# Performance work log

Measured on AMD Instinct MI355X. Metric: run time of the kernel, lower is better.

## Reference

```python
import jax, jax.numpy as jnp
import numpy as np
from jax import lax

# dims
B, CH, CC, DG, H, W = 2, 256, 256, 8, 64, 64
KK = 3  # dcn kernel size
K = KK * KK
GN_GROUPS = 32
EPS = 1e-6


def conv2d(x, w, b, pad=0, groups=1):
    out = lax.conv_general_dilated(x, w, (1, 1), [(pad, pad), (pad, pad)],
                                   feature_group_count=groups)
    return out + b[None, :, None, None]


def group_norm(x, gamma, beta):
    b, c, h, w = x.shape
    xg = x.reshape(b, GN_GROUPS, c // GN_GROUPS, h, w)
    mu = xg.mean(axis=(2, 3, 4), keepdims=True)
    var = xg.var(axis=(2, 3, 4), keepdims=True)
    xn = ((xg - mu) * lax.rsqrt(var + EPS)).reshape(b, c, h, w)
    return xn * gamma[None, :, None, None] + beta[None, :, None, None]


def deform_conv2d(x, off_y, off_x, mask, weight, bias):
    # x: [B,C,H,W]; off_y/off_x/mask: [B,DG,K,H,W]; weight: [Cout,C,3,3]
    b, c, h, w = x.shape
    cg = c // DG
    offs = jnp.arange(KK, dtype=x.dtype) - (KK // 2)  # pad = 1, dilation = 1
    ky = jnp.repeat(offs, KK)  # [K]
    kx = jnp.tile(offs, KK)    # [K]
    base_y = ky[:, None, None] + jnp.arange(h, dtype=x.dtype)[None, :, None]  # [K,H,1]
    base_x = kx[:, None, None] + jnp.arange(w, dtype=x.dtype)[None, None, :]  # [K,1,W]
    py = base_y[None, None] + off_y  # [B,DG,K,H,W]
    px = base_x[None, None] + off_x
    y0f = jnp.floor(py)
    x0f = jnp.floor(px)
    wy1 = py - y0f
    wx1 = px - x0f
    y0 = y0f.astype(jnp.int32)
    x0 = x0f.astype(jnp.int32)
    xg = x.reshape(b, DG, cg, h * w)

    def gather(yi, xi, wt):
        valid = (yi >= 0) & (yi < h) & (xi >= 0) & (xi < w)  # zero padding outside
        idx = (jnp.clip(yi, 0, h - 1) * w + jnp.clip(xi, 0, w - 1)).reshape(b, DG, 1, K * h * w)
        g = jnp.take_along_axis(xg, idx, axis=3).reshape(b, DG, cg, K, h, w)
        return g * (wt * valid)[:, :, None]

    val = (gather(y0, x0, (1 - wy1) * (1 - wx1))
           + gather(y0, x0 + 1, (1 - wy1) * wx1)
           + gather(y0 + 1, x0, wy1 * (1 - wx1))
           + gather(y0 + 1, x0 + 1, wy1 * wx1))
    val = val * mask[:, :, None]  # modulated (DCNv2)
    w_r = weight.reshape(weight.shape[0], DG, cg, K)
    out = jnp.einsum('bgckhw,ogck->bohw', val, w_r)
    return out + bias[None, :, None, None]


def setup_inputs():
    key = jax.random.key(0)
    ks = jax.random.split(key, 32)
    s = 0.02
    inp = {
        'x_main': jax.random.normal(ks[0], (B, CH, H, W), jnp.float32),
        'prior': jax.random.normal(ks[1], (B, CC, 2 * H, 2 * W), jnp.float32),
        # downsample (bilinear resize + 3x3 conv)
        'w_ds': s * jax.random.normal(ks[2], (CC, CC, 3, 3), jnp.float32),
        'b_ds': jnp.zeros((CC,), jnp.float32),
        # offset_conv1: 1x1 -> GN -> SiLU -> depthwise 7x7 -> GN -> SiLU -> 1x1
        'w1': s * jax.random.normal(ks[3], (CH, CH + CC, 1, 1), jnp.float32),
        'b1': jnp.zeros((CH,), jnp.float32),
        'g1': jnp.ones((CH,), jnp.float32),
        'bt1': jnp.zeros((CH,), jnp.float32),
        'w_dw': s * jax.random.normal(ks[4], (CH, 1, 7, 7), jnp.float32),
        'b_dw': jnp.zeros((CH,), jnp.float32),
        'g2': jnp.ones((CH,), jnp.float32),
        'bt2': jnp.zeros((CH,), jnp.float32),
        'w2': s * jax.random.normal(ks[5], (CH, CH, 1, 1), jnp.float32),
        'b2': jnp.zeros((CH,), jnp.float32),
        # offset_conv2: 3x3 -> GN -> SiLU
        'w3': s * jax.random.normal(ks[6], (CH, CH, 3, 3), jnp.float32),
        'b3': jnp.zeros((CH,), jnp.float32),
        'g3': jnp.ones((CH,), jnp.float32),
        'bt3': jnp.zeros((CH,), jnp.float32),
        # dcn.conv_offset: 3x3 -> 3*DG*K channels (small init -> small offsets)
        'w_off': 0.01 * jax.random.normal(ks[7], (3 * DG * K, CH, 3, 3), jnp.float32),
        'b_off': jnp.zeros((3 * DG * K,), jnp.float32),
        # dcn main weight
        'w_dcn': s * jax.random.normal(ks[8], (CH, CH, 3, 3), jnp.float32),
        'b_dcn': jnp.zeros((CH,), jnp.float32),
    }
    return inp


def reference(x_main, prior, w_ds, b_ds, w1, b1, g1, bt1, w_dw, b_dw, g2, bt2,
              w2, b2, w3, b3, g3, bt3, w_off, b_off, w_dcn, b_dcn):
    b, c, h, w = x_main.shape
    # downsample prior to x_main resolution (bilinear, align_corners=False) + 3x3 conv
    pr = jax.image.resize(prior, (b, prior.shape[1], h, w), method='bilinear')
    pr = conv2d(pr, w_ds, b_ds, pad=1)
    # offset_conv1
    t = conv2d(jnp.concatenate([pr, x_main], axis=1), w1, b1, pad=0)
    t = jax.nn.silu(group_norm(t, g1, bt1))
    t = conv2d(t, w_dw, b_dw, pad=3, groups=c)  # depthwise 7x7
    t = jax.nn.silu(group_norm(t, g2, bt2))
    t = conv2d(t, w2, b2, pad=0)
    # offset_conv2 (previous_offset is None)
    offset_feat = jax.nn.silu(group_norm(conv2d(t, w3, b3, pad=1), g3, bt3))
    # DCNv2Pack: offsets/mask from offset_feat, sample x_main
    o = conv2d(offset_feat, w_off, b_off, pad=1)  # [B, 3*DG*K, H, W]
    o1, o2, m = jnp.split(o, 3, axis=1)
    off = jnp.concatenate([o1, o2], axis=1).reshape(b, DG, K, 2, h, w)
    off_y = off[:, :, :, 0]
    off_x = off[:, :, :, 1]
    mask = jax.nn.sigmoid(m).reshape(b, DG, K, h, w)
    warp_feat = deform_conv2d(x_main, off_y, off_x, mask, w_dcn, b_dcn)
    return warp_feat, offset_feat
```

## Files before the change

### kernel.cpp

```cpp
#include <hip/hip_runtime.h>
#include <math.h>


typedef __attribute__((ext_vector_type(8))) short short8;
typedef __attribute__((ext_vector_type(4))) float f32x4;
typedef unsigned short ushort_t;
typedef unsigned int uint_t;

__device__ __forceinline__ ushort_t f2bf(float f) {
  uint_t u = __float_as_uint(f);
  return (ushort_t)((u + 0x7fffu + ((u >> 16) & 1u)) >> 16);
}
__device__ __forceinline__ float bf2f(ushort_t h) {
  return __uint_as_float(((uint_t)h) << 16);
}
__device__ __forceinline__ uint_t pk2(float a, float b) {
  return (uint_t)f2bf(a) | ((uint_t)f2bf(b) << 16);
}

#define GLL(g, l) \
  __builtin_amdgcn_global_load_lds((const __attribute__((address_space(1))) void*)(const void*)(g), \
                                   (__attribute__((address_space(3))) void*)(void*)(l), 16, 0, 0)
#define WAITVM(n) __builtin_amdgcn_s_waitcnt(0x0F70 | (n))
#define CFENCE() asm volatile("" ::: "memory")

#define OFF_P1   0u
#define OFF_Y1   4460544u
#define OFF_Y2   8654848u
#define OFF_O    12849152u
#define OFF_WDS  16388096u
#define OFF_W1   17567744u
#define OFF_W2   17829888u
#define OFF_W3   17960960u
#define OFF_X    19140608u
#define OFF_WDW  23334912u

__global__ __launch_bounds__(256) void k_down(const float* __restrict__ pr,
                                              ushort_t* __restrict__ out) {
  int idx = blockIdx.x * 256 + threadIdx.x;
  int x = idx & 63, y = (idx >> 6) & 63, bc = idx >> 12;
  const float* p = pr + (size_t)bc * 16384;
  const float w4[4] = {0.125f, 0.375f, 0.375f, 0.125f};
  float wy[4], wx[4];
  int ry[4], rx[4];
  float sy = 0.f, sx = 0.f;
#pragma unroll
  for (int t = 0; t < 4; ++t) {
    int yy = 2 * y - 1 + t;
    bool vy = (yy >= 0) && (yy < 128);
    wy[t] = vy ? w4[t] : 0.f; ry[t] = vy ? yy : 0; sy += wy[t];
    int xx = 2 * x - 1 + t;
    bool vx = (xx >= 0) && (xx < 128);
    wx[t] = vx ? w4[t] : 0.f; rx[t] = vx ? xx : 0; sx += wx[t];
  }
  float acc = 0.f;
#pragma unroll
  for (int t = 0; t < 4; ++t) {
    const float* rowp = p + ry[t] * 128;
    acc += wy[t] * (wx[0] * rowp[rx[0]] + wx[1] * rowp[rx[1]] +
                    wx[2] * rowp[rx[2]] + wx[3] * rowp[rx[3]]);
  }
  out[idx] = f2bf(acc / (sy * sx));
}

template <typename SrcT>
__global__ __launch_bounds__(256) void k_tr(const SrcT* __restrict__ src,
                                            ushort_t* __restrict__ dst,
                                            int pad) {
  __shared__ SrcT tile[64][65];
  int bx = blockIdx.x;
  int c4 = bx & 3, y = (bx >> 2) & 63, b = bx >> 8;
  int tid = threadIdx.x;
  int x = tid & 63, cl = tid >> 6;
#pragma unroll
  for (int i = 0; i < 16; ++i) {
    int c = (c4 << 6) + cl + (i << 2);
    tile[cl + (i << 2)][x] = src[(((size_t)(b * 256 + c)) << 12) + (y << 6) + x];
  }
  __syncthreads();
  int W = 64 + 2 * pad;
  int c2 = tid & 63, xq = tid >> 6;
#pragma unroll
  for (int i = 0; i < 16; ++i) {
    int x2 = xq + (i << 2);
    SrcT v = tile[c2][x2];
    ushort_t o;
    if constexpr (sizeof(SrcT) == 4) o = f2bf((float)v); else o = (ushort_t)v;
    dst[((size_t)((b * W + y + pad) * W + x2 + pad)) * 256 + (c4 << 6) + c2] = o;
  }
}

__global__ __launch_bounds__(256) void k_wprep_all(
    const float* __restrict__ w_ds, const float* __restrict__ w1,
    const float* __restrict__ w2, const float* __restrict__ w3,
    const float* __restrict__ w_dw,
    ushort_t* __restrict__ Wds, ushort_t* __restrict__ W1,
    ushort_t* __restrict__ W2, ushort_t* __restrict__ W3,
    float* __restrict__ Wdw) {
  int i = blockIdx.x * 256 + threadIdx.x;
  if (i < 589824) {
    int tap = i >> 16, r = i & 65535, co = r >> 8, ci = r & 255;
    Wds[i] = f2bf(w_ds[((co << 8) + ci) * 9 + tap]);
  } else if (i < 720896) {
    int l = i - 589824;
    W1[l] = f2bf(w1[l]);
  } else if (i < 786432) {
    int l = i - 720896;
    W2[l] = f2bf(w2[l]);
  } else if (i < 1376256) {
    int l = i - 786432;
    int tap = l >> 16, r = l & 65535, co = r >> 8, ci = r & 255;
    W3[l] = f2bf(w3[((co << 8) + ci) * 9 + tap]);
  } else if (i < 1388800) {
    int l = i - 1376256;
    int t = l >> 8, c = l & 255;
    Wdw[l] = w_dw[c * 49 + t];
  }
}

__global__ __launch_bounds__(256) void k_wprep_off(const float* __restrict__ w_off,
                                                   ushort_t* __restrict__ Wof) {
  int i = blockIdx.x * 256 + threadIdx.x;
  int tap = i >> 16, r = i & 65535, co = r >> 8, ci = r & 255;
  Wof[i] = (co < 216) ? f2bf(w_off[((co << 8) + ci) * 9 + tap]) : (ushort_t)0;
}

__global__ __launch_bounds__(256) void k_wdcn(const float* __restrict__ w,
                                              ushort_t* __restrict__ Wd) {
  int i = blockIdx.x * 256 + threadIdx.x;
  int kk = i % 288;
  int rest = i / 288;
  int co = rest & 255, g = rest >> 8;
  int k = kk >> 5, c = kk & 31;
  Wd[i] = f2bf(w[(size_t)co * 2304 + (g * 32 + c) * 9 + k]);
}

template <int NTAPS, int CI>
__global__ __launch_bounds__(256) void k_convmfma(
    const ushort_t* __restrict__ srcA, const ushort_t* __restrict__ srcB,
    const ushort_t* __restrict__ wtp, const float* __restrict__ bias,
    float* __restrict__ outF,
    ushort_t* __restrict__ outB,
    ushort_t* __restrict__ outC16,
    int CO_real, int inH, int inW, int outW, int outPad) {
  const int gx = blockIdx.x;
  const int b = gx >> 6, y = gx & 63;
  const int cobase = blockIdx.y << 7;
  const int tid = threadIdx.x;
  const int wv = tid >> 6, lane = tid & 63;

  __shared__ __align__(16) char lds[36864];

  f32x4 acc[2][4];
#pragma unroll
  for (int mi = 0; mi < 2; ++mi)
#pragma unroll
    for (int ni = 0; ni < 4; ++ni) acc[mi][ni] = (f32x4)0.f;

  const int sub = lane >> 2;
  const int oct = (lane & 3) ^ ((lane >> 3) & 3);

  auto stage = [&](int s, int bufidx) {
    int tap, chunk;
    if constexpr (NTAPS == 9) { tap = s >> 3; chunk = s & 7; }
    else { tap = 0; chunk = s; }
    char* lb = lds + bufidx * 12288;
    {
      int px = (wv << 4) + sub;
      int srow, scol;
      if constexpr (NTAPS == 9) { srow = y + tap / 3; scol = tap % 3 + px; }
      else { srow = y; scol = px; }
      const ushort_t* sp = srcA;
      int cil = chunk << 5;
      if constexpr (CI == 512) {
        if (chunk >= 8) { sp = srcB; cil = (chunk & 7) << 5; }
      }
      const ushort_t* g = sp + ((size_t)((b * inH + srow) * inW + scol) * 256 + cil + (oct << 3));
      GLL(g, lb + (wv << 10));
    }
#pragma unroll
    for (int q = 0; q < 2; ++q) {
      int j = wv + (q << 2);
      int col = (j << 4) + sub;
      const ushort_t* g = wtp + ((size_t)(tap * 256 + cobase + col) * CI + (chunk << 5) + (oct << 3));
      GLL(g, lb + 4096 + (j << 10));
    }
  };

  const int NSTEP = NTAPS * (CI >> 5);
  stage(0, 0);
  stage(1, 1);

  const int r15 = lane & 15;
  const int xo = (((lane >> 4) ^ ((lane >> 1) & 3)) << 4);

  for (int s = 0; s < NSTEP; ++s) {
    if (s + 2 < NSTEP) stage(s + 2, (s + 2) % 3);
    if (s + 2 < NSTEP) WAITVM(6);
    else if (s + 1 < NSTEP) WAITVM(3);
    else WAITVM(0);
    CFENCE();
    __builtin_amdgcn_s_barrier();
    CFENCE();
    char* lb = lds + (s % 3) * 12288;
    short8 af[2];
#pragma unroll
    for (int mi = 0; mi < 2; ++mi)
      af[mi] = *(const short8*)(lb + 4096 + (((wv << 5) + (mi << 4) + r15) << 6) + xo);
#pragma unroll
    for (int ni = 0; ni < 4; ++ni) {
      short8 bfr = *(const short8*)(lb + (((ni << 4) + r15) << 6) + xo);
      acc[0][ni] = __builtin_amdgcn_mfma_f32_16x16x32_bf16(af[0], bfr, acc[0][ni], 0, 0, 0);
      acc[1][ni] = __builtin_amdgcn_mfma_f32_16x16x32_bf16(af[1], bfr, acc[1][ni], 0, 0, 0);
    }
    CFENCE();
    __builtin_amdgcn_s_barrier();
    CFENCE();
  }

  const int coq = (lane >> 4) << 2;
  const int outH = 64 + 2 * outPad;
#pragma unroll
  for (int mi = 0; mi < 2; ++mi) {
    int co4 = cobase + (wv << 5) + (mi << 4) + coq;
    if (co4 >= CO_real) continue;
    float4 bv = *(const float4*)(bias + co4);
#pragma unroll
    for (int ni = 0; ni < 4; ++ni) {
      int px = (ni << 4) + r15;
      f32x4 a = acc[mi][ni];
      if (outF) {
        size_t e = ((size_t)(b * CO_real + co4)) * 4096 + (y << 6) + px;
        outF[e] = a[0] + bv.x;
        outF[e + 4096] = a[1] + bv.y;
        outF[e + 8192] = a[2] + bv.z;
        outF[e + 12288] = a[3] + bv.w;
      }
      if (outC16) {
        size_t e = ((size_t)(b * CO_real + co4)) * 4096 + (y << 6) + px;
        outC16[e] = f2bf(a[0] + bv.x);
        outC16[e + 4096] = f2bf(a[1] + bv.y);
        outC16[e + 8192] = f2bf(a[2] + bv.z);
        outC16[e + 12288] = f2bf(a[3] + bv.w);
      }
      if (outB) {
        size_t e = ((size_t)((b * outH + y + outPad) * outW + px + outPad)) * 256 + co4;
        uint2 u;
        u.x = pk2(a[0] + bv.x, a[1] + bv.y);
        u.y = pk2(a[2] + bv.z, a[3] + bv.w);
        *(uint2*)(outB + e) = u;
      }
    }
  }
}

__global__ __launch_bounds__(256) void k_gn_nhwc(const ushort_t* __restrict__ in,
                                                 ushort_t* __restrict__ outN,
                                                 int outW, int outPad,
                                                 float* __restrict__ outC,
                                                 const float* __restrict__ gamma,
                                                 const float* __restrict__ beta) {
  int bg = blockIdx.x;
  int b = bg >> 5, g = bg & 31, c0 = g << 3;
  const ushort_t* base = in + ((size_t)b * 4096) * 256 + c0;
  int tid = threadIdx.x;

  float s = 0.f, ss = 0.f;
  for (int i = tid; i < 4096; i += 256) {
    uint4 u = *(const uint4*)(base + (size_t)i * 256);
    uint_t w[4] = {u.x, u.y, u.z, u.w};
#pragma unroll
    for (int q = 0; q < 4; ++q) {
      float f0 = __uint_as_float(w[q] << 16);
      float f1 = __uint_as_float(w[q] & 0xffff0000u);
      s += f0 + f1;
      ss += f0 * f0 + f1 * f1;
    }
  }
#pragma unroll
  for (int o = 32; o; o >>= 1) {
    s += __shfl_down(s, o);
    ss += __shfl_down(ss, o);
  }
  __shared__ float rs[4], rss[4], smv[2];
  int wid = tid >> 6;
  if ((tid & 63) == 0) { rs[wid] = s; rss[wid] = ss; }
  __syncthreads();
  if (tid == 0) {
    float S = rs[0] + rs[1] + rs[2] + rs[3];
    float SS = rss[0] + rss[1] + rss[2] + rss[3];
    float mu = S * (1.f / 32768.f);
    float var = SS * (1.f / 32768.f) - mu * mu;
    smv[0] = mu;
    smv[1] = rsqrtf(var + 1e-6f);
  }
  __syncthreads();
  float mu = smv[0], rstd = smv[1];
  float gm[8], bt[8];
#pragma unroll
  for (int j = 0; j < 8; ++j) { gm[j] = gamma[c0 + j]; bt[j] = beta[c0 + j]; }

  for (int i = tid; i < 4096; i += 256) {
    uint4 u = *(const uint4*)(base + (size_t)i * 256);
    uint_t w[4] = {u.x, u.y, u.z, u.w};
    float o8[8];
#pragma unroll
    for (int q = 0; q < 4; ++q) {
      float f0 = __uint_as_float(w[q] << 16);
      float f1 = __uint_as_float(w[q] & 0xffff0000u);
      float v0 = (f0 - mu) * rstd * gm[2 * q] + bt[2 * q];
      float v1 = (f1 - mu) * rstd * gm[2 * q + 1] + bt[2 * q + 1];
      o8[2 * q] = v0 / (1.f + expf(-v0));
      o8[2 * q + 1] = v1 / (1.f + expf(-v1));
    }
    int yy = i >> 6, xx = i & 63;
    size_t e = ((size_t)((b * (64 + 2 * outPad) + yy + outPad) * outW + xx + outPad)) * 256 + c0;
    uint4 o;
    o.x = pk2(o8[0], o8[1]); o.y = pk2(o8[2], o8[3]);
    o.z = pk2(o8[4], o8[5]); o.w = pk2(o8[6], o8[7]);
    *(uint4*)(outN + e) = o;
    if (outC) {
      size_t cb = (((size_t)b << 8) + c0) * 4096 + i;
#pragma unroll
      for (int j = 0; j < 8; ++j) outC[cb + (size_t)j * 4096] = o8[j];
    }
  }
}

__global__ __launch_bounds__(256) void k_dw7_nhwc(const ushort_t* __restrict__ in,
                                                  const float* __restrict__ wdwT,
                                                  const float* __restrict__ bias,
                                                  ushort_t* __restrict__ out) {
  int tid = threadIdx.x;
  int oct = tid & 31, pxl = tid >> 5;
  int pxg = blockIdx.x * 8 + pxl;
  int b = pxg >> 12, rem = pxg & 4095, y = rem >> 6, x = rem & 63;
  float a[8];
  float4 b0 = *(const float4*)(bias + (oct << 3));
  float4 b1 = *(const float4*)(bias + (oct << 3) + 4);
  a[0] = b0.x; a[1] = b0.y; a[2] = b0.z; a[3] = b0.w;
  a[4] = b1.x; a[5] = b1.y; a[6] = b1.z; a[7] = b1.w;
#pragma unroll
  for (int ky = 0; ky < 7; ++ky) {
    int yy = y + ky - 3;
    if ((unsigned)yy >= 64u) continue;
#pragma unroll
    for (int kx = 0; kx < 7; ++kx) {
      int xx = x + kx - 3;
      if ((unsigned)xx >= 64u) continue;
      int t = ky * 7 + kx;
      uint4 u = *(const uint4*)(in + ((size_t)((b << 12) + (yy << 6) + xx)) * 256 + (oct << 3));
      float4 w0 = *(const float4*)(wdwT + (t << 8) + (oct << 3));
      float4 w1 = *(const float4*)(wdwT + (t << 8) + (oct << 3) + 4);
      uint_t ws[4] = {u.x, u.y, u.z, u.w};
      float f[8];
#pragma unroll
      for (int q = 0; q < 4; ++q) {
        f[2 * q] = __uint_as_float(ws[q] << 16);
        f[2 * q + 1] = __uint_as_float(ws[q] & 0xffff0000u);
      }
      a[0] += f[0] * w0.x; a[1] += f[1] * w0.y; a[2] += f[2] * w0.z; a[3] += f[3] * w0.w;
      a[4] += f[4] * w1.x; a[5] += f[5] * w1.y; a[6] += f[6] * w1.z; a[7] += f[7] * w1.w;
    }
  }
  uint4 o;
  o.x = pk2(a[0], a[1]); o.y = pk2(a[2], a[3]);
  o.z = pk2(a[4], a[5]); o.w = pk2(a[6], a[7]);
  *(uint4*)(out + ((size_t)pxg) * 256 + (oct << 3)) = o;
}

__global__ __launch_bounds__(256) void k_dcn_mfma(
    const ushort_t* __restrict__ xb,
    const ushort_t* __restrict__ o16,
    const ushort_t* __restrict__ Wd,
    const float* __restrict__ bias,
    float* __restrict__ out) {
  const int gx = blockIdx.x;
  const int b = gx >> 6, y = gx & 63;
  const int cobase = blockIdx.y << 7;
  const int tid = threadIdx.x;
  const int wv = tid >> 6, lane = tid & 63;
  const int r15 = lane & 15, oct = lane >> 4;

  __shared__ float gw[4][576];
  __shared__ int gi[4][576];
  __shared__ __align__(16) ushort_t val[64][296];

  f32x4 acc[2][4];
#pragma unroll
  for (int mi = 0; mi < 2; ++mi)
#pragma unroll
    for (int ni = 0; ni < 4; ++ni) acc[mi][ni] = (f32x4)0.f;

  const int spx = tid & 63, sc8 = tid >> 6;
  const size_t obase = (size_t)b * 216 * 4096;

  for (int g = 0; g < 8; ++g) {
    __syncthreads();
    for (int t = tid; t < 576; t += 256) {
      int k = t >> 6, px = t & 63;
      int pxy = (y << 6) + px;
      float oy = bf2f(o16[obase + (size_t)(18 * g + 2 * k) * 4096 + pxy]);
      float ox = bf2f(o16[obase + (size_t)(18 * g + 2 * k + 1) * 4096 + pxy]);
      float mm = bf2f(o16[obase + (size_t)(144 + 9 * g + k) * 4096 + pxy]);
      float m = 1.f / (1.f + expf(-mm));
      float py = (float)(y + (k / 3) - 1) + oy;
      float pxf = (float)(px + (k % 3) - 1) + ox;
      float y0f = floorf(py), x0f = floorf(pxf);
      float wy1 = py - y0f, wx1 = pxf - x0f;
      int y0 = (int)y0f, xi0 = (int)x0f;
      int y1 = y0 + 1, xi1 = xi0 + 1;
      float vy0 = (y0 >= 0 && y0 < 64) ? 1.f : 0.f;
      float vy1 = (y1 >= 0 && y1 < 64) ? 1.f : 0.f;
      float vx0 = (xi0 >= 0 && xi0 < 64) ? 1.f : 0.f;
      float vx1 = (xi1 >= 0 && xi1 < 64) ? 1.f : 0.f;
      int y0c = min(max(y0, 0), 63), y1c = min(max(y1, 0), 63);
      int x0c = min(max(xi0, 0), 63), x1c = min(max(xi1, 0), 63);
      float wy0 = 1.f - wy1, wx0 = 1.f - wx1;
      gw[0][t] = wy0 * wx0 * m * vy0 * vx0;
      gw[1][t] = wy0 * wx1 * m * vy0 * vx1;
      gw[2][t] = wy1 * wx0 * m * vy1 * vx0;
      gw[3][t] = wy1 * wx1 * m * vy1 * vx1;
      gi[0][t] = (y0c << 6) + x0c;
      gi[1][t] = (y0c << 6) + x1c;
      gi[2][t] = (y1c << 6) + x0c;
      gi[3][t] = (y1c << 6) + x1c;
    }
    __syncthreads();
    {
      const ushort_t* xg = xb + (((size_t)b << 12) * 256) + (g << 5) + (sc8 << 3);
#pragma unroll
      for (int k = 0; k < 9; ++k) {
        int t = (k << 6) + spx;
        float av[8];
#pragma unroll
        for (int j = 0; j < 8; ++j) av[j] = 0.f;
#pragma unroll
        for (int c4 = 0; c4 < 4; ++c4) {
          float wgt = gw[c4][t];
          uint4 u = *(const uint4*)(xg + (size_t)gi[c4][t] * 256);
          uint_t wsv[4] = {u.x, u.y, u.z, u.w};
#pragma unroll
          for (int q = 0; q < 4; ++q) {
            av[2 * q] += wgt * __uint_as_float(wsv[q] << 16);
            av[2 * q + 1] += wgt * __uint_as_float(wsv[q] & 0xffff0000u);
          }
        }
        uint4 o;
        o.x = pk2(av[0], av[1]); o.y = pk2(av[2], av[3]);
        o.z = pk2(av[4], av[5]); o.w = pk2(av[6], av[7]);
        *(uint4*)(&val[spx][(k << 5) + (sc8 << 3)]) = o;
      }
    }
    __syncthreads();
    const ushort_t* wg = Wd + (size_t)(((g << 8) + cobase + (wv << 5))) * 288;
#pragma unroll
    for (int kc = 0; kc < 9; ++kc) {
      short8 af[2];
#pragma unroll
      for (int mi = 0; mi < 2; ++mi)
        af[mi] = *(const short8*)(wg + (size_t)((mi << 4) + r15) * 288 + (kc << 5) + (oct << 3));
#pragma unroll
      for (int ni = 0; ni < 4; ++ni) {
        short8 bfr = *(const short8*)(&val[(ni << 4) + r15][(kc << 5) + (oct << 3)]);
        acc[0][ni] = __builtin_amdgcn_mfma_f32_16x16x32_bf16(af[0], bfr, acc[0][ni], 0, 0, 0);
        acc[1][ni] = __builtin_amdgcn_mfma_f32_16x16x32_bf16(af[1], bfr, acc[1][ni], 0, 0, 0);
      }
    }
  }
  const int coq = oct << 2;
#pragma unroll
  for (int mi = 0; mi < 2; ++mi) {
    int co4 = cobase + (wv << 5) + (mi << 4) + coq;
    float4 bv = *(const float4*)(bias + co4);
#pragma unroll
    for (int ni = 0; ni < 4; ++ni) {
      int px = (ni << 4) + r15;
      f32x4 a = acc[mi][ni];
      size_t e = (((size_t)b << 8) + co4) * 4096 + (y << 6) + px;
      out[e] = a[0] + bv.x;
      out[e + 4096] = a[1] + bv.y;
      out[e + 8192] = a[2] + bv.z;
      out[e + 12288] = a[3] + bv.w;
    }
  }
}

extern "C" void kernel_launch(void* const* d_in, const int* in_sizes, int n_in,
                              void* d_out, int out_size, void* d_ws,
                              size_t ws_size, hipStream_t stream) {
  const float* x_main = (const float*)d_in[0];
  const float* prior = (const float*)d_in[1];
  const float* w_ds = (const float*)d_in[2];
  const float* b_ds = (const float*)d_in[3];
  const float* w1 = (const float*)d_in[4];
  const float* b1 = (const float*)d_in[5];
  const float* g1 = (const float*)d_in[6];
  const float* bt1 = (const float*)d_in[7];
  const float* w_dw = (const float*)d_in[8];
  const float* b_dw = (const float*)d_in[9];
  const float* g2 = (const float*)d_in[10];
  const float* bt2 = (const float*)d_in[11];
  const float* w2 = (const float*)d_in[12];
  const float* b2 = (const float*)d_in[13];
  const float* w3 = (const float*)d_in[14];
  const float* b3 = (const float*)d_in[15];
  const float* g3 = (const float*)d_in[16];
  const float* bt3 = (const float*)d_in[17];
  const float* w_off = (const float*)d_in[18];
  const float* b_off = (const float*)d_in[19];
  const float* w_dcn = (const float*)d_in[20];
  const float* b_dcn = (const float*)d_in[21];

  float* out = (float*)d_out;
  float* warp = out;
  float* offf = out + 2097152;

  char* ws = (char*)d_ws;
  ushort_t* P1 = (ushort_t*)(ws + OFF_P1);
  ushort_t* Y1 = (ushort_t*)(ws + OFF_Y1);
  ushort_t* Y2 = (ushort_t*)(ws + OFF_Y2);
  ushort_t* o16 = (ushort_t*)(ws + OFF_O);
  ushort_t* Wds = (ushort_t*)(ws + OFF_WDS);
  ushort_t* W1 = (ushort_t*)(ws + OFF_W1);
  ushort_t* W2 = (ushort_t*)(ws + OFF_W2);
  ushort_t* W3 = (ushort_t*)(ws + OFF_W3);
  ushort_t* xb = (ushort_t*)(ws + OFF_X);
  float* Wdw = (float*)(ws + OFF_WDW);
  ushort_t* Wof = Y1;
  ushort_t* Wd = Y1 + 589824;

  hipMemsetAsync(ws + OFF_P1, 0, 4460544, stream);
  k_wprep_all<<<5425, 256, 0, stream>>>(w_ds, w1, w2, w3, w_dw, Wds, W1, W2, W3, Wdw);
  k_down<<<8192, 256, 0, stream>>>(prior, Y2);
  k_tr<ushort_t><<<512, 256, 0, stream>>>(Y2, P1, 1);
  k_tr<float><<<512, 256, 0, stream>>>(x_main, xb, 0);
  k_convmfma<9, 256><<<dim3(128, 2), 256, 0, stream>>>(P1, nullptr, Wds, b_ds,
                                                       nullptr, Y1, nullptr, 256, 66, 66, 64, 0);
  k_convmfma<1, 512><<<dim3(128, 2), 256, 0, stream>>>(Y1, xb, W1, b1,
                                                       nullptr, Y2, nullptr, 256, 64, 64, 64, 0);
  k_gn_nhwc<<<64, 256, 0, stream>>>(Y2, Y1, 64, 0, nullptr, g1, bt1);
  k_dw7_nhwc<<<1024, 256, 0, stream>>>(Y1, Wdw, b_dw, Y2);
  k_gn_nhwc<<<64, 256, 0, stream>>>(Y2, Y1, 64, 0, nullptr, g2, bt2);
  k_convmfma<1, 256><<<dim3(128, 2), 256, 0, stream>>>(Y1, nullptr, W2, b2,
                                                       nullptr, P1, nullptr, 256, 64, 64, 66, 1);
  k_wprep_off<<<2304, 256, 0, stream>>>(w_off, Wof);
  k_wdcn<<<2304, 256, 0, stream>>>(w_dcn, Wd);
  k_convmfma<9, 256><<<dim3(128, 2), 256, 0, stream>>>(P1, nullptr, W3, b3,
                                                       nullptr, Y2, nullptr, 256, 66, 66, 64, 0);
  k_gn_nhwc<<<64, 256, 0, stream>>>(Y2, P1, 66, 1, offf, g3, bt3);
  k_convmfma<9, 256><<<dim3(128, 2), 256, 0, stream>>>(P1, nullptr, Wof, b_off,
                                                       nullptr, nullptr, o16, 216, 66, 66, 64, 0);
  k_dcn_mfma<<<dim3(128, 2), 256, 0, stream>>>(xb, o16, Wd, b_dcn, warp);
}
```

Baseline: 419.2 us.

## Raise grid parallelism: narrower conv tiles, split GroupNorm, re-tiled DCN kernel

The MFMA conv kernel drops from 128 to 64 output channels per block, so each launch has twice as many blocks (grid y 2→4). GroupNorm is split from 64 single-block-per-group launches into a partial-statistics kernel and a row-parallel apply kernel with 128 blocks each. The NCHW float output of offset_feat moves into a separate transpose kernel. The DCN kernel now covers all 256 output channels over half a row per block, with register double-buffered weight fragments, giving 256 blocks. These changes target poor occupancy on a large GPU, at the cost of reloading activations more often and adding extra launches.

Measured after the change: 373.5 us. 1.12x faster.

```diff
diff --git a/kernel.cpp b/kernel.cpp
--- a/kernel.cpp
+++ b/kernel.cpp
@@ -34,6 +34,7 @@
 #define OFF_W3   17960960u
 #define OFF_X    19140608u
 #define OFF_WDW  23334912u
+#define OFF_GNP  23385088u
 
 __global__ __launch_bounds__(256) void k_down(const float* __restrict__ pr,
                                               ushort_t* __restrict__ out) {
@@ -87,6 +88,33 @@
     ushort_t o;
     if constexpr (sizeof(SrcT) == 4) o = f2bf((float)v); else o = (ushort_t)v;
     dst[((size_t)((b * W + y + pad) * W + x2 + pad)) * 256 + (c4 << 6) + c2] = o;
+  }
+}
+
+__global__ __launch_bounds__(256) void k_trnf(const ushort_t* __restrict__ src,
+                                              float* __restrict__ dst) {
+  __shared__ float tile[64][65];
+  int bx = blockIdx.x;
+  int cq = bx & 3, y = (bx >> 2) & 63, b = bx >> 8;
+  int tid = threadIdx.x;
+  int s8 = tid & 7, px = tid >> 3;
+#pragma unroll
+  for (int i = 0; i < 2; ++i) {
+    int p = px + (i << 5);
+    uint4 u = *(const uint4*)(src + ((size_t)((b * 66 + y + 1) * 66 + p + 1)) * 256 + (cq << 6) + (s8 << 3));
+    uint_t w[4] = {u.x, u.y, u.z, u.w};
+#pragma unroll
+    for (int q = 0; q < 4; ++q) {
+      tile[(s8 << 3) + 2 * q][p] = __uint_as_float(w[q] << 16);
+      tile[(s8 << 3) + 2 * q + 1][p] = __uint_as_float(w[q] & 0xffff0000u);
+    }
+  }
+  __syncthreads();
+  int x2 = tid & 63, cl = tid >> 6;
+#pragma unroll
+  for (int i = 0; i < 16; ++i) {
+    int c = cl + (i << 2);
+    dst[((size_t)(b * 256 + (cq << 6) + c)) * 4096 + (y << 6) + x2] = tile[c][x2];
   }
 }
 
@@ -145,17 +173,15 @@
     int CO_real, int inH, int inW, int outW, int outPad) {
   const int gx = blockIdx.x;
   const int b = gx >> 6, y = gx & 63;
-  const int cobase = blockIdx.y << 7;
+  const int cobase = blockIdx.y << 6;
   const int tid = threadIdx.x;
   const int wv = tid >> 6, lane = tid & 63;
 
-  __shared__ __align__(16) char lds[36864];
-
-  f32x4 acc[2][4];
-#pragma unroll
-  for (int mi = 0; mi < 2; ++mi)
-#pragma unroll
-    for (int ni = 0; ni < 4; ++ni) acc[mi][ni] = (f32x4)0.f;
+  __shared__ __align__(16) char lds[24576];
+
+  f32x4 acc[4];
+#pragma unroll
+  for (int ni = 0; ni < 4; ++ni) acc[ni] = (f32x4)0.f;
 
   const int sub = lane >> 2;
   const int oct = (lane & 3) ^ ((lane >> 3) & 3);
@@ -164,7 +190,7 @@
     int tap, chunk;
     if constexpr (NTAPS == 9) { tap = s >> 3; chunk = s & 7; }
     else { tap = 0; chunk = s; }
-    char* lb = lds + bufidx * 12288;
+    char* lb = lds + bufidx * 8192;
     {
       int px = (wv << 4) + sub;
       int srow, scol;
@@ -178,12 +204,10 @@
       const ushort_t* g = sp + ((size_t)((b * inH + srow) * inW + scol) * 256 + cil + (oct << 3));
       GLL(g, lb + (wv << 10));
     }
-#pragma unroll
-    for (int q = 0; q < 2; ++q) {
-      int j = wv + (q << 2);
-      int col = (j << 4) + sub;
+    {
+      int col = (wv << 4) + sub;
       const ushort_t* g = wtp + ((size_t)(tap * 256 + cobase + col) * CI + (chunk << 5) + (oct << 3));
-      GLL(g, lb + 4096 + (j << 10));
+      GLL(g, lb + 4096 + (wv << 10));
     }
   };
 
@@ -196,22 +220,18 @@
 
   for (int s = 0; s < NSTEP; ++s) {
     if (s + 2 < NSTEP) stage(s + 2, (s + 2) % 3);
-    if (s + 2 < NSTEP) WAITVM(6);
-    else if (s + 1 < NSTEP) WAITVM(3);
+    if (s + 2 < NSTEP) WAITVM(4);
+    else if (s + 1 < NSTEP) WAITVM(2);
     else WAITVM(0);
     CFENCE();
     __builtin_amdgcn_s_barrier();
     CFENCE();
-    char* lb = lds + (s % 3) * 12288;
-    short8 af[2];
-#pragma unroll
-    for (int mi = 0; mi < 2; ++mi)
-      af[mi] = *(const short8*)(lb + 4096 + (((wv << 5) + (mi << 4) + r15) << 6) + xo);
+    char* lb = lds + (s % 3) * 8192;
+    short8 af = *(const short8*)(lb + 4096 + (((wv << 4) + r15) << 6) + xo);
 #pragma unroll
     for (int ni = 0; ni < 4; ++ni) {
       short8 bfr = *(const short8*)(lb + (((ni << 4) + r15) << 6) + xo);
-      acc[0][ni] = __builtin_amdgcn_mfma_f32_16x16x32_bf16(af[0], bfr, acc[0][ni], 0, 0, 0);
-      acc[1][ni] = __builtin_amdgcn_mfma_f32_16x16x32_bf16(af[1], bfr, acc[1][ni], 0, 0, 0);
+      acc[ni] = __builtin_amdgcn_mfma_f32_16x16x32_bf16(af, bfr, acc[ni], 0, 0, 0);
     }
     CFENCE();
     __builtin_amdgcn_s_barrier();
@@ -220,15 +240,13 @@
 
   const int coq = (lane >> 4) << 2;
   const int outH = 64 + 2 * outPad;
-#pragma unroll
-  for (int mi = 0; mi < 2; ++mi) {
-    int co4 = cobase + (wv << 5) + (mi << 4) + coq;
-    if (co4 >= CO_real) continue;
+  int co4 = cobase + (wv << 4) + coq;
+  if (co4 < CO_real) {
     float4 bv = *(const float4*)(bias + co4);
 #pragma unroll
     for (int ni = 0; ni < 4; ++ni) {
       int px = (ni << 4) + r15;
-      f32x4 a = acc[mi][ni];
+      f32x4 a = acc[ni];
       if (outF) {
         size_t e = ((size_t)(b * CO_real + co4)) * 4096 + (y << 6) + px;
         outF[e] = a[0] + bv.x;
@@ -254,20 +272,16 @@
   }
 }
 
-__global__ __launch_bounds__(256) void k_gn_nhwc(const ushort_t* __restrict__ in,
-                                                 ushort_t* __restrict__ outN,
-                                                 int outW, int outPad,
-                                                 float* __restrict__ outC,
-                                                 const float* __restrict__ gamma,
-                                                 const float* __restrict__ beta) {
+__global__ __launch_bounds__(256) void k_gnstat(const ushort_t* __restrict__ in,
+                                                float* __restrict__ part) {
   int bg = blockIdx.x;
-  int b = bg >> 5, g = bg & 31, c0 = g << 3;
-  const ushort_t* base = in + ((size_t)b * 4096) * 256 + c0;
   int tid = threadIdx.x;
-
+  int slot = tid & 31, px0 = tid >> 5;
+  const ushort_t* base = in + ((size_t)(bg << 6)) * 256 + (slot << 3);
   float s = 0.f, ss = 0.f;
-  for (int i = tid; i < 4096; i += 256) {
-    uint4 u = *(const uint4*)(base + (size_t)i * 256);
+#pragma unroll
+  for (int i = 0; i < 8; ++i) {
+    uint4 u = *(const uint4*)(base + (size_t)(px0 + (i << 3)) * 256);
     uint_t w[4] = {u.x, u.y, u.z, u.w};
 #pragma unroll
     for (int q = 0; q < 4; ++q) {
@@ -277,31 +291,51 @@
       ss += f0 * f0 + f1 * f1;
     }
   }
-#pragma unroll
-  for (int o = 32; o; o >>= 1) {
-    s += __shfl_down(s, o);
-    ss += __shfl_down(ss, o);
-  }
-  __shared__ float rs[4], rss[4], smv[2];
-  int wid = tid >> 6;
-  if ((tid & 63) == 0) { rs[wid] = s; rss[wid] = ss; }
+  s += __shfl_down(s, 32);
+  ss += __shfl_down(ss, 32);
+  __shared__ float ls[4][32][2];
+  int wv = tid >> 6, lane = tid & 63;
+  if (lane < 32) { ls[wv][lane][0] = s; ls[wv][lane][1] = ss; }
   __syncthreads();
-  if (tid == 0) {
-    float S = rs[0] + rs[1] + rs[2] + rs[3];
-    float SS = rss[0] + rss[1] + rss[2] + rss[3];
-    float mu = S * (1.f / 32768.f);
-    float var = SS * (1.f / 32768.f) - mu * mu;
-    smv[0] = mu;
-    smv[1] = rsqrtf(var + 1e-6f);
+  if (tid < 32) {
+    float S = ls[0][tid][0] + ls[1][tid][0] + ls[2][tid][0] + ls[3][tid][0];
+    float SS = ls[0][tid][1] + ls[1][tid][1] + ls[2][tid][1] + ls[3][tid][1];
+    part[((size_t)bg * 32 + tid) * 2] = S;
+    part[((size_t)bg * 32 + tid) * 2 + 1] = SS;
+  }
+}
+
+__global__ __launch_bounds__(256) void k_gnapply(const ushort_t* __restrict__ in,
+                                                 const float* __restrict__ part,
+                                                 const float* __restrict__ gamma,
+                                                 const float* __restrict__ beta,
+                                                 ushort_t* __restrict__ outN,
+                                                 int outW, int outPad) {
+  int bg = blockIdx.x;
+  int b = bg >> 6, y = bg & 63;
+  int tid = threadIdx.x;
+  __shared__ float stats[32][2];
+  if (tid < 64) {
+    int slot = tid & 31, which = tid >> 5;
+    float a = 0.f;
+    for (int r = 0; r < 64; ++r)
+      a += part[((size_t)(((b << 6) + r) * 32 + slot)) * 2 + which];
+    stats[slot][which] = a;
   }
   __syncthreads();
-  float mu = smv[0], rstd = smv[1];
+  int slot = tid & 31, px0 = tid >> 5;
+  float mu = stats[slot][0] * (1.f / 32768.f);
+  float var = stats[slot][1] * (1.f / 32768.f) - mu * mu;
+  float rstd = rsqrtf(var + 1e-6f);
+  int c0 = slot << 3;
   float gm[8], bt[8];
 #pragma unroll
   for (int j = 0; j < 8; ++j) { gm[j] = gamma[c0 + j]; bt[j] = beta[c0 + j]; }
-
-  for (int i = tid; i < 4096; i += 256) {
-    uint4 u = *(const uint4*)(base + (size_t)i * 256);
+  const ushort_t* base = in + ((size_t)(bg << 6)) * 256 + c0;
+#pragma unroll
+  for (int i = 0; i < 8; ++i) {
+    int px = px0 + (i << 3);
+    uint4 u = *(const uint4*)(base + (size_t)px * 256);
     uint_t w[4] = {u.x, u.y, u.z, u.w};
     float o8[8];
 #pragma unroll
@@ -313,17 +347,11 @@
       o8[2 * q] = v0 / (1.f + expf(-v0));
       o8[2 * q + 1] = v1 / (1.f + expf(-v1));
     }
-    int yy = i >> 6, xx = i & 63;
-    size_t e = ((size_t)((b * (64 + 2 * outPad) + yy + outPad) * outW + xx + outPad)) * 256 + c0;
+    size_t e = ((size_t)((b * (64 + 2 * outPad) + y + outPad) * outW + px + outPad)) * 256 + c0;
     uint4 o;
     o.x = pk2(o8[0], o8[1]); o.y = pk2(o8[2], o8[3]);
     o.z = pk2(o8[4], o8[5]); o.w = pk2(o8[6], o8[7]);
     *(uint4*)(outN + e) = o;
-    if (outC) {
-      size_t cb = (((size_t)b << 8) + c0) * 4096 + i;
-#pragma unroll
-      for (int j = 0; j < 8; ++j) outC[cb + (size_t)j * 4096] = o8[j];
-    }
   }
 }
 
@@ -375,37 +403,41 @@
     const ushort_t* __restrict__ Wd,
     const float* __restrict__ bias,
     float* __restrict__ out) {
-  const int gx = blockIdx.x;
-  const int b = gx >> 6, y = gx & 63;
-  const int cobase = blockIdx.y << 7;
+  const int blk = blockIdx.x;
+  const int b = blk >> 7;
+  const int y = (blk >> 1) & 63;
+  const int xh = blk & 1;
   const int tid = threadIdx.x;
   const int wv = tid >> 6, lane = tid & 63;
   const int r15 = lane & 15, oct = lane >> 4;
 
-  __shared__ float gw[4][576];
-  __shared__ int gi[4][576];
-  __shared__ __align__(16) ushort_t val[64][296];
-
-  f32x4 acc[2][4];
-#pragma unroll
-  for (int mi = 0; mi < 2; ++mi)
-#pragma unroll
-    for (int ni = 0; ni < 4; ++ni) acc[mi][ni] = (f32x4)0.f;
-
-  const int spx = tid & 63, sc8 = tid >> 6;
+  __shared__ float gw[4][288];
+  __shared__ int gi[4][288];
+  __shared__ __align__(16) ushort_t val[32][296];
+
+  f32x4 acc[4][2];
+#pragma unroll
+  for (int mi = 0; mi < 4; ++mi)
+#pragma unroll
+    for (int ni = 0; ni < 2; ++ni) acc[mi][ni] = (f32x4)0.f;
+
+  const int spx = tid & 31;
+  const int sslot = (tid >> 5) & 3;
+  const int skh = tid >> 7;
   const size_t obase = (size_t)b * 216 * 4096;
+  const int pxy0 = (y << 6) + (xh << 5);
 
   for (int g = 0; g < 8; ++g) {
     __syncthreads();
-    for (int t = tid; t < 576; t += 256) {
-      int k = t >> 6, px = t & 63;
-      int pxy = (y << 6) + px;
+    for (int t = tid; t < 288; t += 256) {
+      int k = t >> 5, px = t & 31;
+      int pxy = pxy0 + px;
       float oy = bf2f(o16[obase + (size_t)(18 * g + 2 * k) * 4096 + pxy]);
       float ox = bf2f(o16[obase + (size_t)(18 * g + 2 * k + 1) * 4096 + pxy]);
       float mm = bf2f(o16[obase + (size_t)(144 + 9 * g + k) * 4096 + pxy]);
       float m = 1.f / (1.f + expf(-mm));
       float py = (float)(y + (k / 3) - 1) + oy;
-      float pxf = (float)(px + (k % 3) - 1) + ox;
+      float pxf = (float)((xh << 5) + px + (k % 3) - 1) + ox;
       float y0f = floorf(py), x0f = floorf(pxf);
       float wy1 = py - y0f, wx1 = pxf - x0f;
       int y0 = (int)y0f, xi0 = (int)x0f;
@@ -428,10 +460,9 @@
     }
     __syncthreads();
     {
-      const ushort_t* xg = xb + (((size_t)b << 12) * 256) + (g << 5) + (sc8 << 3);
-#pragma unroll
-      for (int k = 0; k < 9; ++k) {
-        int t = (k << 6) + spx;
+      const ushort_t* xg = xb + (((size_t)b << 12) << 8) + (g << 5) + (sslot << 3);
+      for (int k = skh; k < 9; k += 2) {
+        int t = (k << 5) + spx;
         float av[8];
 #pragma unroll
         for (int j = 0; j < 8; ++j) av[j] = 0.f;
@@ -449,33 +480,41 @@
         uint4 o;
         o.x = pk2(av[0], av[1]); o.y = pk2(av[2], av[3]);
         o.z = pk2(av[4], av[5]); o.w = pk2(av[6], av[7]);
-        *(uint4*)(&val[spx][(k << 5) + (sc8 << 3)]) = o;
+        *(uint4*)(&val[spx][(k << 5) + (sslot << 3)]) = o;
       }
     }
     __syncthreads();
-    const ushort_t* wg = Wd + (size_t)(((g << 8) + cobase + (wv << 5))) * 288;
+    const ushort_t* wg = Wd + ((size_t)((g << 8) + (wv << 6))) * 288;
+    short8 afn[4];
+#pragma unroll
+    for (int mi = 0; mi < 4; ++mi)
+      afn[mi] = *(const short8*)(wg + (size_t)((mi << 4) + r15) * 288 + (oct << 3));
 #pragma unroll
     for (int kc = 0; kc < 9; ++kc) {
-      short8 af[2];
-#pragma unroll
-      for (int mi = 0; mi < 2; ++mi)
-        af[mi] = *(const short8*)(wg + (size_t)((mi << 4) + r15) * 288 + (kc << 5) + (oct << 3));
-#pragma unroll
-      for (int ni = 0; ni < 4; ++ni) {
-        short8 bfr = *(const short8*)(&val[(ni << 4) + r15][(kc << 5) + (oct << 3)]);
-        acc[0][ni] = __builtin_amdgcn_mfma_f32_16x16x32_bf16(af[0], bfr, acc[0][ni], 0, 0, 0);
-        acc[1][ni] = __builtin_amdgcn_mfma_f32_16x16x32_bf16(af[1], bfr, acc[1][ni], 0, 0, 0);
-      }
-    }
-  }
-  const int coq = oct << 2;
-#pragma unroll
-  for (int mi = 0; mi < 2; ++mi) {
-    int co4 = cobase + (wv << 5) + (mi << 4) + coq;
+      short8 afc[4];
+#pragma unroll
+      for (int mi = 0; mi < 4; ++mi) afc[mi] = afn[mi];
+      if (kc < 8) {
+#pragma unroll
+        for (int mi = 0; mi < 4; ++mi)
+          afn[mi] = *(const short8*)(wg + (size_t)((mi << 4) + r15) * 288 + ((kc + 1) << 5) + (oct << 3));
+      }
+      short8 bf0 = *(const short8*)(&val[r15][(kc << 5) + (oct << 3)]);
+      short8 bf1 = *(const short8*)(&val[16 + r15][(kc << 5) + (oct << 3)]);
+#pragma unroll
+      for (int mi = 0; mi < 4; ++mi) {
+        acc[mi][0] = __builtin_amdgcn_mfma_f32_16x16x32_bf16(afc[mi], bf0, acc[mi][0], 0, 0, 0);
+        acc[mi][1] = __builtin_amdgcn_mfma_f32_16x16x32_bf16(afc[mi], bf1, acc[mi][1], 0, 0, 0);
+      }
+    }
+  }
+#pragma unroll
+  for (int mi = 0; mi < 4; ++mi) {
+    int co4 = (wv << 6) + (mi << 4) + (oct << 2);
     float4 bv = *(const float4*)(bias + co4);
 #pragma unroll
-    for (int ni = 0; ni < 4; ++ni) {
-      int px = (ni << 4) + r15;
+    for (int ni = 0; ni < 2; ++ni) {
+      int px = (xh << 5) + (ni << 4) + r15;
       f32x4 a = acc[mi][ni];
       size_t e = (((size_t)b << 8) + co4) * 4096 + (y << 6) + px;
       out[e] = a[0] + bv.x;
@@ -527,6 +566,7 @@
   ushort_t* W3 = (ushort_t*)(ws + OFF_W3);
   ushort_t* xb = (ushort_t*)(ws + OFF_X);
   float* Wdw = (float*)(ws + OFF_WDW);
+  float* gnp = (float*)(ws + OFF_GNP);
   ushort_t* Wof = Y1;
   ushort_t* Wd = Y1 + 589824;
 
@@ -535,21 +575,25 @@
   k_down<<<8192, 256, 0, stream>>>(prior, Y2);
   k_tr<ushort_t><<<512, 256, 0, stream>>>(Y2, P1, 1);
   k_tr<float><<<512, 256, 0, stream>>>(x_main, xb, 0);
-  k_convmfma<9, 256><<<dim3(128, 2), 256, 0, stream>>>(P1, nullptr, Wds, b_ds,
+  k_convmfma<9, 256><<<dim3(128, 4), 256, 0, stream>>>(P1, nullptr, Wds, b_ds,
                                                        nullptr, Y1, nullptr, 256, 66, 66, 64, 0);
-  k_convmfma<1, 512><<<dim3(128, 2), 256, 0, stream>>>(Y1, xb, W1, b1,
+  k_convmfma<1, 512><<<dim3(128, 4), 256, 0, stream>>>(Y1, xb, W1, b1,
                                                        nullptr, Y2, nullptr, 256, 64, 64, 64, 0);
-  k_gn_nhwc<<<64, 256, 0, stream>>>(Y2, Y1, 64, 0, nullptr, g1, bt1);
+  k_gnstat<<<128, 256, 0, stream>>>(Y2, gnp);
+  k_gnapply<<<128, 256, 0, stream>>>(Y2, gnp, g1, bt1, Y1, 64, 0);
   k_dw7_nhwc<<<1024, 256, 0, stream>>>(Y1, Wdw, b_dw, Y2);
-  k_gn_nhwc<<<64, 256, 0, stream>>>(Y2, Y1, 64, 0, nullptr, g2, bt2);
-  k_convmfma<1, 256><<<dim3(128, 2), 256, 0, stream>>>(Y1, nullptr, W2, b2,
+  k_gnstat<<<128, 256, 0, stream>>>(Y2, gnp);
+  k_gnapply<<<128, 256, 0, stream>>>(Y2, gnp, g2, bt2, Y1, 64, 0);
+  k_convmfma<1, 256><<<dim3(128, 4), 256, 0, stream>>>(Y1, nullptr, W2, b2,
                                                        nullptr, P1, nullptr, 256, 64, 64, 66, 1);
   k_wprep_off<<<2304, 256, 0, stream>>>(w_off, Wof);
   k_wdcn<<<2304, 256, 0, stream>>>(w_dcn, Wd);
-  k_convmfma<9, 256><<<dim3(128, 2), 256, 0, stream>>>(P1, nullptr, W3, b3,
+  k_convmfma<9, 256><<<dim3(128, 4), 256, 0, stream>>>(P1, nullptr, W3, b3,
                                                        nullptr, Y2, nullptr, 256, 66, 66, 64, 0);
-  k_gn_nhwc<<<64, 256, 0, stream>>>(Y2, P1, 66, 1, offf, g3, bt3);
-  k_convmfma<9, 256><<<dim3(128, 2), 256, 0, stream>>>(P1, nullptr, Wof, b_off,
+  k_gnstat<<<128, 256, 0, stream>>>(Y2, gnp);
+  k_gnapply<<<128, 256, 0, stream>>>(Y2, gnp, g3, bt3, P1, 66, 1);
+  k_trnf<<<512, 256, 0, stream>>>(P1, offf);
+  k_convmfma<9, 256><<<dim3(128, 4), 256, 0, stream>>>(P1, nullptr, Wof, b_off,
                                                        nullptr, nullptr, o16, 216, 66, 66, 64, 0);
-  k_dcn_mfma<<<dim3(128, 2), 256, 0, stream>>>(xb, o16, Wd, b_dcn, warp);
-}
+  k_dcn_mfma<<<256, 256, 0, stream>>>(xb, o16, Wd, b_dcn, warp);
+}
```
